# Kernel tuning notes

Hardware: AMD Instinct MI355X
Metric: run time of the kernel (lower is better)

## Reference

```python
import jax, jax.numpy as jnp
import numpy as np

M, N, K = 4096, 8192, 4096


def setup_inputs() -> dict:
    key = jax.random.key(0)
    k1, k2, k3, k4 = jax.random.split(key, 4)
    a = jax.random.randint(k1, (M, K), 0, 127, dtype=jnp.int32)  # int8 activations
    b = jax.random.randint(k2, (N, K), 0, 127, dtype=jnp.int32)  # int8 weights (row-major [N,K])
    alpha_row = jax.random.uniform(k3, (M, 1), dtype=jnp.float16)  # per-row dequant scale
    alpha_col = jax.random.uniform(k4, (1, N), dtype=jnp.float16)  # per-col dequant scale
    return {"a": a, "b": b, "alpha_row": alpha_row, "alpha_col": alpha_col}


def reference(a, b, alpha_row, alpha_col):
    # x = a @ b.T in fp32 (int8 values upcast), then rescale by outer product of scales
    x = jnp.matmul(a.astype(jnp.float32), b.astype(jnp.float32).T)  # [M, N]
    scale = alpha_row.astype(jnp.float32) * alpha_col.astype(jnp.float32)  # [M, N] via broadcast
    out = x * scale
    return out.astype(jnp.float16)
```

## Files before the change

kernel.cpp:

```cpp
#include <hip/hip_runtime.h>
#include <cstdint>
#include <cstddef>

#define M_DIM 4096
#define N_DIM 8192
#define K_DIM 4096

typedef __attribute__((ext_vector_type(4))) int int4v;

__global__ void __launch_bounds__(256) pack_frag(const int* __restrict__ a,
                                                 const int* __restrict__ b,
                                                 unsigned char* __restrict__ pa,
                                                 unsigned char* __restrict__ pb) {
    size_t t = (size_t)blockIdx.x * 256 + threadIdx.x;
    const size_t NA = (size_t)(M_DIM / 16) * (K_DIM / 64) * 64;
    const int* __restrict__ src;
    unsigned char* __restrict__ dst;
    if (t < NA) {
        src = a; dst = pa;
    } else {
        src = b; dst = pb; t -= NA;
    }
    const int l = (int)(t & 63);
    const int s = (int)((t >> 6) & 63);
    const int p = (int)(t >> 12);
    const int* g = src + ((size_t)(16 * p + (l & 15))) * K_DIM + s * 64 + (l >> 4) * 16;
    const int4v* g4 = (const int4v*)g;
    int4v o;
#pragma unroll
    for (int q = 0; q < 4; ++q) {
        int4v v = g4[q];
        o[q] = (v[0] & 0xff) | ((v[1] & 0xff) << 8) | ((v[2] & 0xff) << 16) | (v[3] << 24);
    }
    ((int4v*)dst)[t] = o;
}

__device__ inline void async_copy16(const unsigned char* g, unsigned char* l) {
    __builtin_amdgcn_global_load_lds(
        (const __attribute__((address_space(1))) void*)g,
        (__attribute__((address_space(3))) void*)l,
        16, 0, 0);
}

#define BAR() __builtin_amdgcn_s_barrier()

__global__ void __launch_bounds__(512, 2) gemm_i8(const unsigned char* __restrict__ Ap,
                                                  const unsigned char* __restrict__ Bp,
                                                  const _Float16* __restrict__ arow,
                                                  const _Float16* __restrict__ acol,
                                                  _Float16* __restrict__ Cout) {
    __shared__ __align__(16) unsigned char lds[4 * 32768];

    const int tid  = threadIdx.x;
    const int lane = tid & 63;
    const int wave = tid >> 6;
    const int wr   = wave >> 2;
    const int wc   = wave & 3;
    const int bn   = blockIdx.x;
    const int bm   = blockIdx.y;

    const unsigned char* aP0 = Ap + (size_t)(bm * 16 + 2 * wave) * 65536 + lane * 16;
    const unsigned char* aP1 = aP0 + 65536;
    const unsigned char* bP0 = Bp + (size_t)(bn * 16 + 2 * wave) * 65536 + lane * 16;
    const unsigned char* bP1 = bP0 + 65536;
    const int aL0 = 2 * wave * 1024, aL1 = aL0 + 1024;
    const int bL0 = 16384 + 2 * wave * 1024, bL1 = bL0 + 1024;

#define STAGE(lo)                                  \
    do {                                           \
        async_copy16(aP0, lds + (lo) + aL0);       \
        async_copy16(aP1, lds + (lo) + aL1);       \
        async_copy16(bP0, lds + (lo) + bL0);       \
        async_copy16(bP1, lds + (lo) + bL1);       \
        aP0 += 1024; aP1 += 1024;                  \
        bP0 += 1024; bP1 += 1024;                  \
    } while (0)

    const int a_off = wr * 8192 + lane * 16;
    const int b_off = 16384 + wc * 4096 + lane * 16;

    int4v acc[8][4];
#pragma unroll
    for (int i = 0; i < 8; ++i)
#pragma unroll
        for (int j = 0; j < 4; ++j) acc[i][j] = (int4v)0;

    const int NT = K_DIM / 64;

    STAGE(0);
    STAGE(32768);
    STAGE(65536);
    asm volatile("s_waitcnt vmcnt(4)" ::: "memory");
    BAR();

    int4v bf0[4], bf1[4];
#pragma unroll
    for (int j = 0; j < 4; ++j) bf0[j] = *(const int4v*)(lds + b_off + j * 1024);

#pragma unroll 1
    for (int u = 0; u < NT / 2; ++u) {
        {
            const int T = 2 * u;
            if (T + 3 < NT) STAGE(((T + 3) & 3) * 32768);
            const unsigned char* Ac = lds + (T & 3) * 32768;
            const unsigned char* Bn = lds + ((T + 1) & 3) * 32768;
            int4v af[8];
#pragma unroll
            for (int i = 0; i < 8; ++i) af[i] = *(const int4v*)(Ac + a_off + i * 1024);
#pragma unroll
            for (int j = 0; j < 4; ++j) bf1[j] = *(const int4v*)(Bn + b_off + j * 1024);
#pragma unroll
            for (int i = 0; i < 8; ++i)
#pragma unroll
                for (int j = 0; j < 4; ++j)
                    acc[i][j] = __builtin_amdgcn_mfma_i32_16x16x64_i8(af[i], bf0[j],
                                                                      acc[i][j], 0, 0, 0);
            if (T + 3 < NT) {
                asm volatile("s_waitcnt vmcnt(4)" ::: "memory");
            } else {
                asm volatile("s_waitcnt vmcnt(0)" ::: "memory");
            }
            BAR();
        }
        {
            const int T = 2 * u + 1;
            if (T + 3 < NT) STAGE(((T + 3) & 3) * 32768);
            const unsigned char* Ac = lds + (T & 3) * 32768;
            int4v af[8];
#pragma unroll
            for (int i = 0; i < 8; ++i) af[i] = *(const int4v*)(Ac + a_off + i * 1024);
            if (T + 1 < NT) {
                const unsigned char* Bn = lds + ((T + 1) & 3) * 32768;
#pragma unroll
                for (int j = 0; j < 4; ++j) bf0[j] = *(const int4v*)(Bn + b_off + j * 1024);
            }
#pragma unroll
            for (int i = 0; i < 8; ++i)
#pragma unroll
                for (int j = 0; j < 4; ++j)
                    acc[i][j] = __builtin_amdgcn_mfma_i32_16x16x64_i8(af[i], bf1[j],
                                                                      acc[i][j], 0, 0, 0);
            if (T + 3 < NT) {
                asm volatile("s_waitcnt vmcnt(4)" ::: "memory");
            } else {
                asm volatile("s_waitcnt vmcnt(0)" ::: "memory");
            }
            BAR();
        }
    }
#undef STAGE

    const int gcol0 = bn * 256 + wc * 64 + (lane & 15);
    float ac4[4];
#pragma unroll
    for (int j = 0; j < 4; ++j) ac4[j] = (float)acol[gcol0 + j * 16];

    const size_t grow0 = (size_t)bm * 256 + wr * 128 + (lane >> 4) * 4;
#pragma unroll
    for (int i = 0; i < 8; ++i) {
#pragma unroll
        for (int r = 0; r < 4; ++r) {
            const size_t row = grow0 + i * 16 + r;
            const float ar = (float)arow[row];
            _Float16* outp = Cout + row * (size_t)N_DIM + gcol0;
#pragma unroll
            for (int j = 0; j < 4; ++j) {
                float v = (float)acc[i][j][r] * ar * ac4[j];
                outp[j * 16] = (_Float16)v;
            }
        }
    }
}

extern "C" void kernel_launch(void* const* d_in, const int* in_sizes, int n_in,
                              void* d_out, int out_size, void* d_ws, size_t ws_size,
                              hipStream_t stream) {
    const int* a = (const int*)d_in[0];
    const int* b = (const int*)d_in[1];
    const _Float16* ar = (const _Float16*)d_in[2];
    const _Float16* ac = (const _Float16*)d_in[3];
    _Float16* out = (_Float16*)d_out;

    unsigned char* pa = (unsigned char*)d_ws;
    unsigned char* pb = pa + (size_t)M_DIM * K_DIM;

    const size_t total_frag = (size_t)(M_DIM / 16 + N_DIM / 16) * (K_DIM / 64) * 64;
    pack_frag<<<(int)(total_frag / 256), 256, 0, stream>>>(a, b, pa, pb);

    dim3 grid(N_DIM / 256, M_DIM / 256);
    gemm_i8<<<grid, 512, 0, stream>>>(pa, pb, ar, ac, out);
}
```

Measured before the change: 367.0 us.

## Load B fragments directly into registers and stage only A through LDS

B tiles no longer go through LDS. Each wave now loads its own four B fragments straight from global memory into registers, one K-step ahead. Only A is staged through a three-buffer LDS ring, which shrinks shared memory from 128KB to 48KB and removes the B LDS reads. The explicit vmcnt waits are dropped, so the code relies on compiler-inserted waits for the B register loads to also cover the earlier async A copies. Global traffic for B roughly doubles because waves in the same column duplicate the loads, and the synchronisation is now fragile.

```diff
diff --git a/kernel.cpp b/kernel.cpp
--- a/kernel.cpp
+++ b/kernel.cpp
@@ -49,7 +49,7 @@
                                                   const _Float16* __restrict__ arow,
                                                   const _Float16* __restrict__ acol,
                                                   _Float16* __restrict__ Cout) {
-    __shared__ __align__(16) unsigned char lds[4 * 32768];
+    __shared__ __align__(16) unsigned char lds[3 * 16384];
 
     const int tid  = threadIdx.x;
     const int lane = tid & 63;
@@ -61,23 +61,29 @@
 
     const unsigned char* aP0 = Ap + (size_t)(bm * 16 + 2 * wave) * 65536 + lane * 16;
     const unsigned char* aP1 = aP0 + 65536;
-    const unsigned char* bP0 = Bp + (size_t)(bn * 16 + 2 * wave) * 65536 + lane * 16;
+    const int aL0 = 2 * wave * 1024;
+    const int aL1 = aL0 + 1024;
+
+#define STAGE_A(lo)                          \
+    do {                                     \
+        async_copy16(aP0, lds + (lo) + aL0); \
+        async_copy16(aP1, lds + (lo) + aL1); \
+        aP0 += 1024; aP1 += 1024;            \
+    } while (0)
+
+    const unsigned char* bP0 = Bp + (size_t)(bn * 16 + wc * 4) * 65536 + lane * 16;
     const unsigned char* bP1 = bP0 + 65536;
-    const int aL0 = 2 * wave * 1024, aL1 = aL0 + 1024;
-    const int bL0 = 16384 + 2 * wave * 1024, bL1 = bL0 + 1024;
+    const unsigned char* bP2 = bP0 + 2 * 65536;
+    const unsigned char* bP3 = bP0 + 3 * 65536;
 
-#define STAGE(lo)                                  \
-    do {                                           \
-        async_copy16(aP0, lds + (lo) + aL0);       \
-        async_copy16(aP1, lds + (lo) + aL1);       \
-        async_copy16(bP0, lds + (lo) + bL0);       \
-        async_copy16(bP1, lds + (lo) + bL1);       \
-        aP0 += 1024; aP1 += 1024;                  \
-        bP0 += 1024; bP1 += 1024;                  \
+#define LOAD_B(dst)                                                  \
+    do {                                                             \
+        dst[0] = *(const int4v*)bP0; dst[1] = *(const int4v*)bP1;    \
+        dst[2] = *(const int4v*)bP2; dst[3] = *(const int4v*)bP3;    \
+        bP0 += 1024; bP1 += 1024; bP2 += 1024; bP3 += 1024;          \
     } while (0)
 
     const int a_off = wr * 8192 + lane * 16;
-    const int b_off = 16384 + wc * 4096 + lane * 16;
 
     int4v acc[8][4];
 #pragma unroll
@@ -86,69 +92,58 @@
         for (int j = 0; j < 4; ++j) acc[i][j] = (int4v)0;
 
     const int NT = K_DIM / 64;
+    const int NU = NT / 2;
 
-    STAGE(0);
-    STAGE(32768);
-    STAGE(65536);
+    STAGE_A(0);
+    STAGE_A(16384);
+    int4v bf0[4], bf1[4];
+    LOAD_B(bf0);
     asm volatile("s_waitcnt vmcnt(4)" ::: "memory");
     BAR();
 
-    int4v bf0[4], bf1[4];
-#pragma unroll
-    for (int j = 0; j < 4; ++j) bf0[j] = *(const int4v*)(lds + b_off + j * 1024);
+    int o_cur = 0, o_nxt = 16384, o_pre = 32768;
 
 #pragma unroll 1
-    for (int u = 0; u < NT / 2; ++u) {
+    for (int u = 0; u < NU; ++u) {
         {
-            const int T = 2 * u;
-            if (T + 3 < NT) STAGE(((T + 3) & 3) * 32768);
-            const unsigned char* Ac = lds + (T & 3) * 32768;
-            const unsigned char* Bn = lds + ((T + 1) & 3) * 32768;
+            if (u < NU - 1) STAGE_A(o_pre);
+            LOAD_B(bf1);
+            const unsigned char* Ac = lds + o_cur;
             int4v af[8];
 #pragma unroll
             for (int i = 0; i < 8; ++i) af[i] = *(const int4v*)(Ac + a_off + i * 1024);
-#pragma unroll
-            for (int j = 0; j < 4; ++j) bf1[j] = *(const int4v*)(Bn + b_off + j * 1024);
+            asm volatile("" ::: "memory");
 #pragma unroll
             for (int i = 0; i < 8; ++i)
 #pragma unroll
                 for (int j = 0; j < 4; ++j)
                     acc[i][j] = __builtin_amdgcn_mfma_i32_16x16x64_i8(af[i], bf0[j],
                                                                       acc[i][j], 0, 0, 0);
-            if (T + 3 < NT) {
-                asm volatile("s_waitcnt vmcnt(4)" ::: "memory");
-            } else {
-                asm volatile("s_waitcnt vmcnt(0)" ::: "memory");
-            }
             BAR();
+            const int t0 = o_cur; o_cur = o_nxt; o_nxt = o_pre; o_pre = t0;
         }
         {
-            const int T = 2 * u + 1;
-            if (T + 3 < NT) STAGE(((T + 3) & 3) * 32768);
-            const unsigned char* Ac = lds + (T & 3) * 32768;
+            if (u < NU - 1) {
+                STAGE_A(o_pre);
+                LOAD_B(bf0);
+            }
+            const unsigned char* Ac = lds + o_cur;
             int4v af[8];
 #pragma unroll
             for (int i = 0; i < 8; ++i) af[i] = *(const int4v*)(Ac + a_off + i * 1024);
-            if (T + 1 < NT) {
-                const unsigned char* Bn = lds + ((T + 1) & 3) * 32768;
-#pragma unroll
-                for (int j = 0; j < 4; ++j) bf0[j] = *(const int4v*)(Bn + b_off + j * 1024);
-            }
+            asm volatile("" ::: "memory");
 #pragma unroll
             for (int i = 0; i < 8; ++i)
 #pragma unroll
                 for (int j = 0; j < 4; ++j)
                     acc[i][j] = __builtin_amdgcn_mfma_i32_16x16x64_i8(af[i], bf1[j],
                                                                       acc[i][j], 0, 0, 0);
-            if (T + 3 < NT) {
-                asm volatile("s_waitcnt vmcnt(4)" ::: "memory");
-            } else {
-                asm volatile("s_waitcnt vmcnt(0)" ::: "memory");
-            }
             BAR();
+            const int t0 = o_cur; o_cur = o_nxt; o_nxt = o_pre; o_pre = t0;
         }
     }
-#undef STAGE
+#undef STAGE_A
+#undef LOAD_B
 
     const int gcol0 = bn * 256 + wc * 64 + (lane & 15);
     float ac4[4];
```

After: 383.6 us. 4.5% more time.

## Stagger MFMA phases across wave groups with triple-buffered LDS pipeline

Applied to the files above, without the earlier changes.

Reduces the LDS ring from four stages to three and removes the B-fragment register double-buffering. Waves in the second row group (wr==1) run their MFMA cluster for the previous tile at the top of the next iteration, so the two wave groups alternate between LDS reads and MFMA work. The goal is to spread LDS traffic over time and stop all waves contending for LDS at once, while also lowering LDS use per block. The shallower prefetch depth may expose more global-load latency, and the skewed schedule holds af/bf registers across the barrier.

```diff
diff --git a/kernel.cpp b/kernel.cpp
--- a/kernel.cpp
+++ b/kernel.cpp
@@ -49,13 +49,14 @@
                                                   const _Float16* __restrict__ arow,
                                                   const _Float16* __restrict__ acol,
                                                   _Float16* __restrict__ Cout) {
-    __shared__ __align__(16) unsigned char lds[4 * 32768];
+    __shared__ __align__(16) unsigned char lds[3 * 32768];
 
     const int tid  = threadIdx.x;
     const int lane = tid & 63;
     const int wave = tid >> 6;
     const int wr   = wave >> 2;
     const int wc   = wave & 3;
+    const bool isB = (wr == 1);
     const int bn   = blockIdx.x;
     const int bm   = blockIdx.y;
 
@@ -89,66 +90,45 @@
 
     STAGE(0);
     STAGE(32768);
-    STAGE(65536);
     asm volatile("s_waitcnt vmcnt(4)" ::: "memory");
     BAR();
 
-    int4v bf0[4], bf1[4];
-#pragma unroll
-    for (int j = 0; j < 4; ++j) bf0[j] = *(const int4v*)(lds + b_off + j * 1024);
+    int4v af[8], bf[4];
+
+#define MFMA_CLUSTER()                                                          \
+    do {                                                                        \
+        _Pragma("unroll")                                                       \
+        for (int i = 0; i < 8; ++i)                                             \
+            _Pragma("unroll")                                                   \
+            for (int j = 0; j < 4; ++j)                                         \
+                acc[i][j] = __builtin_amdgcn_mfma_i32_16x16x64_i8(af[i], bf[j], \
+                                                                  acc[i][j], 0, 0, 0); \
+    } while (0)
 
 #pragma unroll 1
-    for (int u = 0; u < NT / 2; ++u) {
-        {
-            const int T = 2 * u;
-            if (T + 3 < NT) STAGE(((T + 3) & 3) * 32768);
-            const unsigned char* Ac = lds + (T & 3) * 32768;
-            const unsigned char* Bn = lds + ((T + 1) & 3) * 32768;
-            int4v af[8];
+    for (int T = 0; T < NT; ++T) {
+        if (isB && T > 0) MFMA_CLUSTER();
+
+        if (T + 2 < NT) STAGE(((T + 2) % 3) * 32768);
+
+        const unsigned char* Ac = lds + (T % 3) * 32768;
 #pragma unroll
-            for (int i = 0; i < 8; ++i) af[i] = *(const int4v*)(Ac + a_off + i * 1024);
+        for (int i = 0; i < 8; ++i) af[i] = *(const int4v*)(Ac + a_off + i * 1024);
 #pragma unroll
-            for (int j = 0; j < 4; ++j) bf1[j] = *(const int4v*)(Bn + b_off + j * 1024);
-#pragma unroll
-            for (int i = 0; i < 8; ++i)
-#pragma unroll
-                for (int j = 0; j < 4; ++j)
-                    acc[i][j] = __builtin_amdgcn_mfma_i32_16x16x64_i8(af[i], bf0[j],
-                                                                      acc[i][j], 0, 0, 0);
-            if (T + 3 < NT) {
-                asm volatile("s_waitcnt vmcnt(4)" ::: "memory");
-            } else {
-                asm volatile("s_waitcnt vmcnt(0)" ::: "memory");
-            }
-            BAR();
+        for (int j = 0; j < 4; ++j) bf[j] = *(const int4v*)(Ac + b_off + j * 1024);
+
+        if (!isB) MFMA_CLUSTER();
+
+        if (T + 2 < NT) {
+            asm volatile("s_waitcnt vmcnt(4)" ::: "memory");
+        } else {
+            asm volatile("s_waitcnt vmcnt(0)" ::: "memory");
         }
-        {
-            const int T = 2 * u + 1;
-            if (T + 3 < NT) STAGE(((T + 3) & 3) * 32768);
-            const unsigned char* Ac = lds + (T & 3) * 32768;
-            int4v af[8];
-#pragma unroll
-            for (int i = 0; i < 8; ++i) af[i] = *(const int4v*)(Ac + a_off + i * 1024);
-            if (T + 1 < NT) {
-                const unsigned char* Bn = lds + ((T + 1) & 3) * 32768;
-#pragma unroll
-                for (int j = 0; j < 4; ++j) bf0[j] = *(const int4v*)(Bn + b_off + j * 1024);
-            }
-#pragma unroll
-            for (int i = 0; i < 8; ++i)
-#pragma unroll
-                for (int j = 0; j < 4; ++j)
-                    acc[i][j] = __builtin_amdgcn_mfma_i32_16x16x64_i8(af[i], bf1[j],
-                                                                      acc[i][j], 0, 0, 0);
-            if (T + 3 < NT) {
-                asm volatile("s_waitcnt vmcnt(4)" ::: "memory");
-            } else {
-                asm volatile("s_waitcnt vmcnt(0)" ::: "memory");
-            }
-            BAR();
-        }
+        BAR();
     }
+    if (isB) MFMA_CLUSTER();
 #undef STAGE
+#undef MFMA_CLUSTER
 
     const int gcol0 = bn * 256 + wc * 64 + (lane & 15);
     float ac4[4];
```

Measured after the change: 357.9 us. 2.5% less time.
